# Kernel optimization log

Hardware: AMD Instinct MI355X
Metric: run time of the kernel (lower is better)

The kernel has to match this reference:

```python
import jax, jax.numpy as jnp
import numpy as np

NUM_E = 200000   # number of entities/nodes
HID = 128        # hidsize
N_EDGES = 600000


def setup_inputs() -> dict:
    key = jax.random.key(0)
    k1, k2, k3, k4, k5, k6 = jax.random.split(key, 6)
    emb = jax.random.normal(k1, (NUM_E, HID), dtype=jnp.float32)
    edge_id = jax.random.randint(k2, (2, N_EDGES), 0, NUM_E, dtype=jnp.int64)
    edge_w = jax.random.uniform(k3, (N_EDGES,), dtype=jnp.float32)
    # MGCNConvLayer params (diag=True => diagonal/vector weights)
    w_diag = jax.random.normal(k4, (HID,), dtype=jnp.float32) * 0.1   # neighbor-path diag weight
    loop_w = jax.random.normal(k5, (HID,), dtype=jnp.float32) * 0.1   # jump/self-loop diag weight (isjump=True)
    bias = jnp.zeros((HID,), dtype=jnp.float32)
    res = jnp.asarray([0.1], dtype=jnp.float32)                       # StateHistory residual scale
    return {"emb": emb, "edge_id": edge_id, "edge_w": edge_w,
            "w_diag": w_diag, "loop_w": loop_w, "bias": bias, "res": res}


def reference(emb, edge_id, edge_w, w_diag, loop_w, bias, res):
    # --- MGCNConvLayer.forward(emb, edge_id, rel=None, num_e, dN=edge_w) ---
    src = edge_id[0]
    dst = edge_id[1]
    # gather source embeddings, weight by per-edge dN, scatter-add to destinations
    msg = emb[src] * edge_w[:, None]                       # [E, HID]
    agg = jax.ops.segment_sum(msg, dst, num_segments=NUM_E)  # [N, HID]
    # diagonal transform of aggregated messages + jump (self) path + bias, then act
    h = jnp.tanh(agg * w_diag + emb * loop_w + bias)        # [N, HID]
    # --- StateHistory tail: scaled residual; dropout is identity in eval ---
    tmp = res * h                                           # res broadcasts ([1])
    out = emb + tmp
    return (out, tmp)
```

## Files before the change

### kernel.cpp

```cpp
#include <hip/hip_runtime.h>

constexpr int NUM_E   = 200000;
constexpr int HID     = 128;
constexpr int N_EDGES = 600000;
constexpr int CAP     = 24;

typedef float    floatx4 __attribute__((ext_vector_type(4)));
typedef float    floatx8 __attribute__((ext_vector_type(8)));
typedef int      intx4   __attribute__((ext_vector_type(4)));
typedef _Float16 halfx4  __attribute__((ext_vector_type(4)));
typedef _Float16 halfx8  __attribute__((ext_vector_type(8)));


__global__ __launch_bounds__(256) void zero_cursor_kernel(int* __restrict__ cursor)
{
    int i = blockIdx.x * blockDim.x + threadIdx.x;
    if (i < NUM_E / 4) reinterpret_cast<intx4*>(cursor)[i] = (intx4)(0);
}

__global__ __launch_bounds__(256) void convert_zero_kernel(
    const float* __restrict__ emb, halfx8* __restrict__ embh8,
    int* __restrict__ cursor)
{
    int i = blockIdx.x * blockDim.x + threadIdx.x;
    constexpr int total = NUM_E * HID / 8;
    if (i < NUM_E / 4) reinterpret_cast<intx4*>(cursor)[i] = (intx4)(0);
    if (i >= total) return;
    const floatx4* e4 = reinterpret_cast<const floatx4*>(emb) + (size_t)i * 2;
    floatx4 v0 = e4[0], v1 = e4[1];
    floatx8 v  = __builtin_shufflevector(v0, v1, 0, 1, 2, 3, 4, 5, 6, 7);
    embh8[i] = __builtin_convertvector(v, halfx8);
}

__global__ __launch_bounds__(256) void binning_kernel(
    const int* __restrict__ edge_id, const float* __restrict__ edge_w,
    int* __restrict__ cursor, int2* __restrict__ pairs)
{
    int e = blockIdx.x * blockDim.x + threadIdx.x;
    if (e < N_EDGES) {
        int d    = edge_id[N_EDGES + e];
        int slot = atomicAdd(&cursor[d], 1);
        if (slot < CAP)
            pairs[(size_t)d * CAP + slot] = make_int2(edge_id[e], __float_as_int(edge_w[e]));
    }
}

__global__ __launch_bounds__(256) void gather_epilogue_h_kernel(
    const float*  __restrict__ emb,
    const halfx4* __restrict__ embh4,
    const int*    __restrict__ cursor,
    const int2*   __restrict__ pairs,
    const float*  __restrict__ w_diag,
    const float*  __restrict__ loop_w,
    const float*  __restrict__ bias,
    const float*  __restrict__ res,
    float*        __restrict__ out,
    float*        __restrict__ tmp)
{
    int t = blockIdx.x * blockDim.x + threadIdx.x;
    constexpr int total = NUM_E * 8;
    if (t >= total) return;
    int n = t >> 3;
    int c = t & 7;

    int deg = cursor[n];
    if (deg > CAP) deg = CAP;
    const int2* pb = pairs + (size_t)n * CAP;

    floatx4 a0 = (floatx4)(0.f);
    floatx4 a1 = (floatx4)(0.f);
    floatx4 a2 = (floatx4)(0.f);
    floatx4 a3 = (floatx4)(0.f);

    int k = 0;
    for (; k + 2 <= deg; k += 2) {
        int2 p0 = pb[k];
        int2 p1 = pb[k + 1];
        float w0 = __int_as_float(p0.y);
        float w1 = __int_as_float(p1.y);
        const halfx4* r0 = embh4 + (size_t)p0.x * (HID / 4);
        const halfx4* r1 = embh4 + (size_t)p1.x * (HID / 4);
        halfx4 h00 = r0[c], h01 = r0[c + 8], h02 = r0[c + 16], h03 = r0[c + 24];
        halfx4 h10 = r1[c], h11 = r1[c + 8], h12 = r1[c + 16], h13 = r1[c + 24];
        a0 += __builtin_convertvector(h00, floatx4) * w0;
        a1 += __builtin_convertvector(h01, floatx4) * w0;
        a2 += __builtin_convertvector(h02, floatx4) * w0;
        a3 += __builtin_convertvector(h03, floatx4) * w0;
        a0 += __builtin_convertvector(h10, floatx4) * w1;
        a1 += __builtin_convertvector(h11, floatx4) * w1;
        a2 += __builtin_convertvector(h12, floatx4) * w1;
        a3 += __builtin_convertvector(h13, floatx4) * w1;
    }
    if (k < deg) {
        int2 p0 = pb[k];
        float w0 = __int_as_float(p0.y);
        const halfx4* r0 = embh4 + (size_t)p0.x * (HID / 4);
        a0 += __builtin_convertvector(r0[c],      floatx4) * w0;
        a1 += __builtin_convertvector(r0[c + 8],  floatx4) * w0;
        a2 += __builtin_convertvector(r0[c + 16], floatx4) * w0;
        a3 += __builtin_convertvector(r0[c + 24], floatx4) * w0;
    }

    const float r = res[0];
    const floatx4* emb4 = reinterpret_cast<const floatx4*>(emb);
    const floatx4* wd4  = reinterpret_cast<const floatx4*>(w_diag);
    const floatx4* lw4  = reinterpret_cast<const floatx4*>(loop_w);
    const floatx4* bb4  = reinterpret_cast<const floatx4*>(bias);
    floatx4* out4 = reinterpret_cast<floatx4*>(out);
    floatx4* tmp4 = reinterpret_cast<floatx4*>(tmp);
    const size_t base = (size_t)n * (HID / 4);

    floatx4 acc[4] = {a0, a1, a2, a3};
#pragma unroll
    for (int j = 0; j < 4; ++j) {
        int    cc  = c + 8 * j;
        size_t idx = base + cc;
        floatx4 ev = emb4[idx];
        floatx4 wd = wd4[cc], lw = lw4[cc], bb = bb4[cc];
        floatx4 tm, o;
        tm.x = r * tanhf(fmaf(acc[j].x, wd.x, fmaf(ev.x, lw.x, bb.x)));
        tm.y = r * tanhf(fmaf(acc[j].y, wd.y, fmaf(ev.y, lw.y, bb.y)));
        tm.z = r * tanhf(fmaf(acc[j].z, wd.z, fmaf(ev.z, lw.z, bb.z)));
        tm.w = r * tanhf(fmaf(acc[j].w, wd.w, fmaf(ev.w, lw.w, bb.w)));
        o = ev + tm;
        __builtin_nontemporal_store(o,  out4 + idx);
        __builtin_nontemporal_store(tm, tmp4 + idx);
    }
}

__global__ __launch_bounds__(256) void gather_epilogue_kernel(
    const float* __restrict__ emb,
    const int*   __restrict__ cursor,
    const int2*  __restrict__ pairs,
    const float* __restrict__ w_diag,
    const float* __restrict__ loop_w,
    const float* __restrict__ bias,
    const float* __restrict__ res,
    float*       __restrict__ out,
    float*       __restrict__ tmp)
{
    int t = blockIdx.x * blockDim.x + threadIdx.x;
    constexpr int total = NUM_E * 8;
    if (t >= total) return;
    int n = t >> 3;
    int c = t & 7;

    const floatx4* emb4 = reinterpret_cast<const floatx4*>(emb);
    int deg = cursor[n];
    if (deg > CAP) deg = CAP;
    const int2* pb = pairs + (size_t)n * CAP;

    floatx4 a0 = (floatx4)(0.f), a1 = (floatx4)(0.f);
    floatx4 a2 = (floatx4)(0.f), a3 = (floatx4)(0.f);

    int k = 0;
    for (; k + 2 <= deg; k += 2) {
        int2 p0 = pb[k], p1 = pb[k + 1];
        float w0 = __int_as_float(p0.y), w1 = __int_as_float(p1.y);
        const floatx4* r0 = emb4 + (size_t)p0.x * (HID / 4);
        const floatx4* r1 = emb4 + (size_t)p1.x * (HID / 4);
        a0 += r0[c] * w0;  a1 += r0[c + 8] * w0;  a2 += r0[c + 16] * w0;  a3 += r0[c + 24] * w0;
        a0 += r1[c] * w1;  a1 += r1[c + 8] * w1;  a2 += r1[c + 16] * w1;  a3 += r1[c + 24] * w1;
    }
    if (k < deg) {
        int2 p0 = pb[k];
        float w0 = __int_as_float(p0.y);
        const floatx4* r0 = emb4 + (size_t)p0.x * (HID / 4);
        a0 += r0[c] * w0;  a1 += r0[c + 8] * w0;  a2 += r0[c + 16] * w0;  a3 += r0[c + 24] * w0;
    }

    const float r = res[0];
    const floatx4* wd4 = reinterpret_cast<const floatx4*>(w_diag);
    const floatx4* lw4 = reinterpret_cast<const floatx4*>(loop_w);
    const floatx4* bb4 = reinterpret_cast<const floatx4*>(bias);
    floatx4* out4 = reinterpret_cast<floatx4*>(out);
    floatx4* tmp4 = reinterpret_cast<floatx4*>(tmp);
    const size_t base = (size_t)n * (HID / 4);

    floatx4 acc[4] = {a0, a1, a2, a3};
#pragma unroll
    for (int j = 0; j < 4; ++j) {
        int    cc  = c + 8 * j;
        size_t idx = base + cc;
        floatx4 ev = emb4[idx];
        floatx4 wd = wd4[cc], lw = lw4[cc], bb = bb4[cc];
        floatx4 tm, o;
        tm.x = r * tanhf(fmaf(acc[j].x, wd.x, fmaf(ev.x, lw.x, bb.x)));
        tm.y = r * tanhf(fmaf(acc[j].y, wd.y, fmaf(ev.y, lw.y, bb.y)));
        tm.z = r * tanhf(fmaf(acc[j].z, wd.z, fmaf(ev.z, lw.z, bb.z)));
        tm.w = r * tanhf(fmaf(acc[j].w, wd.w, fmaf(ev.w, lw.w, bb.w)));
        o = ev + tm;
        __builtin_nontemporal_store(o,  out4 + idx);
        __builtin_nontemporal_store(tm, tmp4 + idx);
    }
}

extern "C" void kernel_launch(void* const* d_in, const int* in_sizes, int n_in,
                              void* d_out, int out_size, void* d_ws, size_t ws_size,
                              hipStream_t stream) {
    const float* emb     = (const float*)d_in[0];
    const int*   edge_id = (const int*)  d_in[1];
    const float* edge_w  = (const float*)d_in[2];
    const float* w_diag  = (const float*)d_in[3];
    const float* loop_w  = (const float*)d_in[4];
    const float* bias    = (const float*)d_in[5];
    const float* res     = (const float*)d_in[6];

    float* out = (float*)d_out;
    float* tmp = out + (size_t)NUM_E * HID;

    int*    cursor = (int*)d_ws;
    int2*   pairs  = (int2*)(cursor + NUM_E);
    halfx8* embh8  = (halfx8*)(pairs + (size_t)NUM_E * CAP);
    halfx4* embh4  = (halfx4*)embh8;

    const size_t need_h = (size_t)NUM_E * 4 + (size_t)NUM_E * CAP * 8
                        + (size_t)NUM_E * HID * 2;

    if (ws_size >= need_h) {
        convert_zero_kernel<<<(NUM_E * HID / 8 + 255) / 256, 256, 0, stream>>>(
            emb, embh8, cursor);
        binning_kernel<<<(N_EDGES + 255) / 256, 256, 0, stream>>>(
            edge_id, edge_w, cursor, pairs);
        gather_epilogue_h_kernel<<<(NUM_E * 8 + 255) / 256, 256, 0, stream>>>(
            emb, embh4, cursor, pairs, w_diag, loop_w, bias, res, out, tmp);
    } else {
        zero_cursor_kernel<<<(NUM_E / 4 + 255) / 256, 256, 0, stream>>>(cursor);
        binning_kernel<<<(N_EDGES + 255) / 256, 256, 0, stream>>>(
            edge_id, edge_w, cursor, pairs);
        gather_epilogue_kernel<<<(NUM_E * 8 + 255) / 256, 256, 0, stream>>>(
            emb, cursor, pairs, w_diag, loop_w, bias, res, out, tmp);
    }
}
```

Before: 129.6 us.

## Map one wavefront per node in fp16 gather and read self embedding from fp16

The gather/epilogue kernel now assigns 64 threads per node, each accumulating two fp16 columns, so each neighbor row is read as a single coalesced 256-byte access per wave. The epilogue reads the node's own embedding from the fp16 copy instead of the fp32 input, cutting read traffic. The conversion kernel uses nontemporal loads. The costs are more threads, smaller per-thread loads, repeated pair-list reads across lanes, and fp16 rounding now entering the out = emb + tmp output.

```diff
diff --git a/kernel.cpp b/kernel.cpp
--- a/kernel.cpp
+++ b/kernel.cpp
@@ -5,10 +5,11 @@
 constexpr int N_EDGES = 600000;
 constexpr int CAP     = 24;
 
+typedef float    floatx2 __attribute__((ext_vector_type(2)));
 typedef float    floatx4 __attribute__((ext_vector_type(4)));
 typedef float    floatx8 __attribute__((ext_vector_type(8)));
 typedef int      intx4   __attribute__((ext_vector_type(4)));
-typedef _Float16 halfx4  __attribute__((ext_vector_type(4)));
+typedef _Float16 halfx2  __attribute__((ext_vector_type(2)));
 typedef _Float16 halfx8  __attribute__((ext_vector_type(8)));
 
 
@@ -27,7 +28,8 @@
     if (i < NUM_E / 4) reinterpret_cast<intx4*>(cursor)[i] = (intx4)(0);
     if (i >= total) return;
     const floatx4* e4 = reinterpret_cast<const floatx4*>(emb) + (size_t)i * 2;
-    floatx4 v0 = e4[0], v1 = e4[1];
+    floatx4 v0 = __builtin_nontemporal_load(e4);
+    floatx4 v1 = __builtin_nontemporal_load(e4 + 1);
     floatx8 v  = __builtin_shufflevector(v0, v1, 0, 1, 2, 3, 4, 5, 6, 7);
     embh8[i] = __builtin_convertvector(v, halfx8);
 }
@@ -45,9 +47,8 @@
     }
 }
 
-__global__ __launch_bounds__(256) void gather_epilogue_h_kernel(
-    const float*  __restrict__ emb,
-    const halfx4* __restrict__ embh4,
+__global__ __launch_bounds__(256) void gather_epilogue_h64_kernel(
+    const halfx2* __restrict__ embh2,
     const int*    __restrict__ cursor,
     const int2*   __restrict__ pairs,
     const float*  __restrict__ w_diag,
@@ -57,55 +58,98 @@
     float*        __restrict__ out,
     float*        __restrict__ tmp)
 {
-    int t = blockIdx.x * blockDim.x + threadIdx.x;
-    constexpr int total = NUM_E * 8;
+    long long t = (long long)blockIdx.x * blockDim.x + threadIdx.x;
+    constexpr long long total = (long long)NUM_E * 64;
     if (t >= total) return;
-    int n = t >> 3;
-    int c = t & 7;
+    int n    = (int)(t >> 6);
+    int lane = (int)(t & 63);
 
     int deg = cursor[n];
     if (deg > CAP) deg = CAP;
     const int2* pb = pairs + (size_t)n * CAP;
 
-    floatx4 a0 = (floatx4)(0.f);
-    floatx4 a1 = (floatx4)(0.f);
-    floatx4 a2 = (floatx4)(0.f);
-    floatx4 a3 = (floatx4)(0.f);
-
+    floatx2 acc = (floatx2)(0.f);
     int k = 0;
     for (; k + 2 <= deg; k += 2) {
         int2 p0 = pb[k];
         int2 p1 = pb[k + 1];
         float w0 = __int_as_float(p0.y);
         float w1 = __int_as_float(p1.y);
-        const halfx4* r0 = embh4 + (size_t)p0.x * (HID / 4);
-        const halfx4* r1 = embh4 + (size_t)p1.x * (HID / 4);
-        halfx4 h00 = r0[c], h01 = r0[c + 8], h02 = r0[c + 16], h03 = r0[c + 24];
-        halfx4 h10 = r1[c], h11 = r1[c + 8], h12 = r1[c + 16], h13 = r1[c + 24];
-        a0 += __builtin_convertvector(h00, floatx4) * w0;
-        a1 += __builtin_convertvector(h01, floatx4) * w0;
-        a2 += __builtin_convertvector(h02, floatx4) * w0;
-        a3 += __builtin_convertvector(h03, floatx4) * w0;
-        a0 += __builtin_convertvector(h10, floatx4) * w1;
-        a1 += __builtin_convertvector(h11, floatx4) * w1;
-        a2 += __builtin_convertvector(h12, floatx4) * w1;
-        a3 += __builtin_convertvector(h13, floatx4) * w1;
+        halfx2 h0 = embh2[(size_t)p0.x * 64 + lane];
+        halfx2 h1 = embh2[(size_t)p1.x * 64 + lane];
+        acc += __builtin_convertvector(h0, floatx2) * w0;
+        acc += __builtin_convertvector(h1, floatx2) * w1;
     }
     if (k < deg) {
         int2 p0 = pb[k];
         float w0 = __int_as_float(p0.y);
-        const halfx4* r0 = embh4 + (size_t)p0.x * (HID / 4);
-        a0 += __builtin_convertvector(r0[c],      floatx4) * w0;
-        a1 += __builtin_convertvector(r0[c + 8],  floatx4) * w0;
-        a2 += __builtin_convertvector(r0[c + 16], floatx4) * w0;
-        a3 += __builtin_convertvector(r0[c + 24], floatx4) * w0;
+        halfx2 h0 = embh2[(size_t)p0.x * 64 + lane];
+        acc += __builtin_convertvector(h0, floatx2) * w0;
     }
 
     const float r = res[0];
+    const size_t idx = (size_t)n * 64 + lane;
+    floatx2 ev = __builtin_convertvector(embh2[idx], floatx2);
+    floatx2 wd = reinterpret_cast<const floatx2*>(w_diag)[lane];
+    floatx2 lw = reinterpret_cast<const floatx2*>(loop_w)[lane];
+    floatx2 bb = reinterpret_cast<const floatx2*>(bias)[lane];
+
+    floatx2 tm, o;
+    tm.x = r * tanhf(fmaf(acc.x, wd.x, fmaf(ev.x, lw.x, bb.x)));
+    tm.y = r * tanhf(fmaf(acc.y, wd.y, fmaf(ev.y, lw.y, bb.y)));
+    o = ev + tm;
+
+    floatx2* out2 = reinterpret_cast<floatx2*>(out);
+    floatx2* tmp2 = reinterpret_cast<floatx2*>(tmp);
+    __builtin_nontemporal_store(o,  out2 + idx);
+    __builtin_nontemporal_store(tm, tmp2 + idx);
+}
+
+__global__ __launch_bounds__(256) void gather_epilogue_kernel(
+    const float* __restrict__ emb,
+    const int*   __restrict__ cursor,
+    const int2*  __restrict__ pairs,
+    const float* __restrict__ w_diag,
+    const float* __restrict__ loop_w,
+    const float* __restrict__ bias,
+    const float* __restrict__ res,
+    float*       __restrict__ out,
+    float*       __restrict__ tmp)
+{
+    int t = blockIdx.x * blockDim.x + threadIdx.x;
+    constexpr int total = NUM_E * 8;
+    if (t >= total) return;
+    int n = t >> 3;
+    int c = t & 7;
+
     const floatx4* emb4 = reinterpret_cast<const floatx4*>(emb);
-    const floatx4* wd4  = reinterpret_cast<const floatx4*>(w_diag);
-    const floatx4* lw4  = reinterpret_cast<const floatx4*>(loop_w);
-    const floatx4* bb4  = reinterpret_cast<const floatx4*>(bias);
+    int deg = cursor[n];
+    if (deg > CAP) deg = CAP;
+    const int2* pb = pairs + (size_t)n * CAP;
+
+    floatx4 a0 = (floatx4)(0.f), a1 = (floatx4)(0.f);
+    floatx4 a2 = (floatx4)(0.f), a3 = (floatx4)(0.f);
+
+    int k = 0;
+    for (; k + 2 <= deg; k += 2) {
+        int2 p0 = pb[k], p1 = pb[k + 1];
+        float w0 = __int_as_float(p0.y), w1 = __int_as_float(p1.y);
+        const floatx4* r0 = emb4 + (size_t)p0.x * (HID / 4);
+        const floatx4* r1 = emb4 + (size_t)p1.x * (HID / 4);
+        a0 += r0[c] * w0;  a1 += r0[c + 8] * w0;  a2 += r0[c + 16] * w0;  a3 += r0[c + 24] * w0;
+        a0 += r1[c] * w1;  a1 += r1[c + 8] * w1;  a2 += r1[c + 16] * w1;  a3 += r1[c + 24] * w1;
+    }
+    if (k < deg) {
+        int2 p0 = pb[k];
+        float w0 = __int_as_float(p0.y);
+        const floatx4* r0 = emb4 + (size_t)p0.x * (HID / 4);
+        a0 += r0[c] * w0;  a1 += r0[c + 8] * w0;  a2 += r0[c + 16] * w0;  a3 += r0[c + 24] * w0;
+    }
+
+    const float r = res[0];
+    const floatx4* wd4 = reinterpret_cast<const floatx4*>(w_diag);
+    const floatx4* lw4 = reinterpret_cast<const floatx4*>(loop_w);
+    const floatx4* bb4 = reinterpret_cast<const floatx4*>(bias);
     floatx4* out4 = reinterpret_cast<floatx4*>(out);
     floatx4* tmp4 = reinterpret_cast<floatx4*>(tmp);
     const size_t base = (size_t)n * (HID / 4);
@@ -128,73 +172,6 @@
     }
 }
 
-__global__ __launch_bounds__(256) void gather_epilogue_kernel(
-    const float* __restrict__ emb,
-    const int*   __restrict__ cursor,
-    const int2*  __restrict__ pairs,
-    const float* __restrict__ w_diag,
-    const float* __restrict__ loop_w,
-    const float* __restrict__ bias,
-    const float* __restrict__ res,
-    float*       __restrict__ out,
-    float*       __restrict__ tmp)
-{
-    int t = blockIdx.x * blockDim.x + threadIdx.x;
-    constexpr int total = NUM_E * 8;
-    if (t >= total) return;
-    int n = t >> 3;
-    int c = t & 7;
-
-    const floatx4* emb4 = reinterpret_cast<const floatx4*>(emb);
-    int deg = cursor[n];
-    if (deg > CAP) deg = CAP;
-    const int2* pb = pairs + (size_t)n * CAP;
-
-    floatx4 a0 = (floatx4)(0.f), a1 = (floatx4)(0.f);
-    floatx4 a2 = (floatx4)(0.f), a3 = (floatx4)(0.f);
-
-    int k = 0;
-    for (; k + 2 <= deg; k += 2) {
-        int2 p0 = pb[k], p1 = pb[k + 1];
-        float w0 = __int_as_float(p0.y), w1 = __int_as_float(p1.y);
-        const floatx4* r0 = emb4 + (size_t)p0.x * (HID / 4);
-        const floatx4* r1 = emb4 + (size_t)p1.x * (HID / 4);
-        a0 += r0[c] * w0;  a1 += r0[c + 8] * w0;  a2 += r0[c + 16] * w0;  a3 += r0[c + 24] * w0;
-        a0 += r1[c] * w1;  a1 += r1[c + 8] * w1;  a2 += r1[c + 16] * w1;  a3 += r1[c + 24] * w1;
-    }
-    if (k < deg) {
-        int2 p0 = pb[k];
-        float w0 = __int_as_float(p0.y);
-        const floatx4* r0 = emb4 + (size_t)p0.x * (HID / 4);
-        a0 += r0[c] * w0;  a1 += r0[c + 8] * w0;  a2 += r0[c + 16] * w0;  a3 += r0[c + 24] * w0;
-    }
-
-    const float r = res[0];
-    const floatx4* wd4 = reinterpret_cast<const floatx4*>(w_diag);
-    const floatx4* lw4 = reinterpret_cast<const floatx4*>(loop_w);
-    const floatx4* bb4 = reinterpret_cast<const floatx4*>(bias);
-    floatx4* out4 = reinterpret_cast<floatx4*>(out);
-    floatx4* tmp4 = reinterpret_cast<floatx4*>(tmp);
-    const size_t base = (size_t)n * (HID / 4);
-
-    floatx4 acc[4] = {a0, a1, a2, a3};
-#pragma unroll
-    for (int j = 0; j < 4; ++j) {
-        int    cc  = c + 8 * j;
-        size_t idx = base + cc;
-        floatx4 ev = emb4[idx];
-        floatx4 wd = wd4[cc], lw = lw4[cc], bb = bb4[cc];
-        floatx4 tm, o;
-        tm.x = r * tanhf(fmaf(acc[j].x, wd.x, fmaf(ev.x, lw.x, bb.x)));
-        tm.y = r * tanhf(fmaf(acc[j].y, wd.y, fmaf(ev.y, lw.y, bb.y)));
-        tm.z = r * tanhf(fmaf(acc[j].z, wd.z, fmaf(ev.z, lw.z, bb.z)));
-        tm.w = r * tanhf(fmaf(acc[j].w, wd.w, fmaf(ev.w, lw.w, bb.w)));
-        o = ev + tm;
-        __builtin_nontemporal_store(o,  out4 + idx);
-        __builtin_nontemporal_store(tm, tmp4 + idx);
-    }
-}
-
 extern "C" void kernel_launch(void* const* d_in, const int* in_sizes, int n_in,
                               void* d_out, int out_size, void* d_ws, size_t ws_size,
                               hipStream_t stream) {
@@ -212,7 +189,7 @@
     int*    cursor = (int*)d_ws;
     int2*   pairs  = (int2*)(cursor + NUM_E);
     halfx8* embh8  = (halfx8*)(pairs + (size_t)NUM_E * CAP);
-    halfx4* embh4  = (halfx4*)embh8;
+    halfx2* embh2  = (halfx2*)embh8;
 
     const size_t need_h = (size_t)NUM_E * 4 + (size_t)NUM_E * CAP * 8
                         + (size_t)NUM_E * HID * 2;
@@ -222,8 +199,9 @@
             emb, embh8, cursor);
         binning_kernel<<<(N_EDGES + 255) / 256, 256, 0, stream>>>(
             edge_id, edge_w, cursor, pairs);
-        gather_epilogue_h_kernel<<<(NUM_E * 8 + 255) / 256, 256, 0, stream>>>(
-            emb, embh4, cursor, pairs, w_diag, loop_w, bias, res, out, tmp);
+        long long total = (long long)NUM_E * 64;
+        gather_epilogue_h64_kernel<<<(int)((total + 255) / 256), 256, 0, stream>>>(
+            embh2, cursor, pairs, w_diag, loop_w, bias, res, out, tmp);
     } else {
         zero_cursor_kernel<<<(NUM_E / 4 + 255) / 256, 256, 0, stream>>>(cursor);
         binning_kernel<<<(N_EDGES + 255) / 256, 256, 0, stream>>>(
```

New measurement: 139.9 us. 8.0% more time.
